# Performance work log

Measured on AMD Instinct MI355X. Metric: run time of the kernel, lower is better.

The kernel has to match this reference:

```python
import jax, jax.numpy as jnp
import numpy as np

SOFTCAP = 50.0
EPS = 1e-6
N_HEADS, D_HEAD = 16, 64


def _rms(x, w):
    return x * jax.lax.rsqrt(jnp.mean(x * x, axis=-1, keepdims=True) + EPS) * w


def _rope(x, cos, sin):
    # Faithful to source: apply_rope uses x.size(1) as the position axis, but is
    # called on (B, H, T, Dh) tensors, so positions are indexed by HEAD index.
    n = x.shape[1]
    x1, x2 = x[..., 0::2], x[..., 1::2]
    c = cos[:n][None, :, None, :]
    s = sin[:n][None, :, None, :]
    return jnp.stack([x1 * c - x2 * s, x1 * s + x2 * c], axis=-1).reshape(x.shape)


def setup_inputs() -> dict:
    key = jax.random.key(0)
    ks = jax.random.split(key, 12)
    L, D, H, Dh, Dff, V, B, T = 6, 1024, N_HEADS, D_HEAD, 4096, 32000, 1, 1024
    r = lambda k, shape: jax.random.normal(k, shape, dtype=jnp.float32) * 0.02
    return {
        'x': jax.random.randint(ks[0], (B, T), 0, V, dtype=jnp.int32),
        'embed': r(ks[1], (V, D)),
        'ln1': jnp.ones((L, D), jnp.float32),
        'Wq': r(ks[2], (L, H * Dh, D)),
        'Wk': r(ks[3], (L, H * Dh, D)),
        'Wv': r(ks[4], (L, H * Dh, D)),
        'Wo': r(ks[5], (L, D, H * Dh)),
        'qn': jnp.ones((L, Dh), jnp.float32),
        'kn': jnp.ones((L, Dh), jnp.float32),
        'ln2': jnp.ones((L, D), jnp.float32),
        'Wg': r(ks[6], (L, Dff, D)),
        'Wu': r(ks[7], (L, Dff, D)),
        'Wd': r(ks[8], (L, D, Dff)),
        'ln_out': jnp.ones((D,), jnp.float32),
    }


def reference(x, embed, ln1, Wq, Wk, Wv, Wo, qn, kn, ln2, Wg, Wu, Wd, ln_out):
    B, T = x.shape
    H, Dh = N_HEADS, D_HEAD
    scale = Dh ** -0.5
    # RoPE tables (theta=10000)
    freqs = 1.0 / (10000.0 ** (jnp.arange(0, Dh, 2, dtype=jnp.float32) / Dh))
    ang = jnp.arange(T, dtype=jnp.float32)[:, None] * freqs[None, :]
    cos, sin = jnp.cos(ang), jnp.sin(ang)
    mask = jnp.triu(jnp.ones((T, T), dtype=bool), k=1)  # True above diagonal

    h = embed[x]  # (B, T, D)

    def block(h, p):
        l1, wq, wk, wv, wo, qnw, knw, l2, wg, wu, wd = p
        hn = _rms(h, l1)
        q = (hn @ wq.T).reshape(B, T, H, Dh).transpose(0, 2, 1, 3)  # (B,H,T,Dh)
        k = (hn @ wk.T).reshape(B, T, H, Dh).transpose(0, 2, 1, 3)
        v = (hn @ wv.T).reshape(B, T, H, Dh).transpose(0, 2, 1, 3)
        q = _rope(_rms(q, qnw), cos, sin)
        k = _rope(_rms(k, knw), cos, sin)
        scores = jnp.einsum('bhtd,bhsd->bhts', q, k) * scale
        scores = SOFTCAP * jnp.tanh(scores / SOFTCAP)
        scores = jnp.where(mask[None, None], -jnp.inf, scores)
        attn = jax.nn.softmax(scores, axis=-1)
        o = jnp.einsum('bhts,bhsd->bhtd', attn, v)
        o = o.transpose(0, 2, 1, 3).reshape(B, T, H * Dh)
        h = h + o @ wo.T
        hn2 = _rms(h, l2)
        h = h + (jax.nn.silu(hn2 @ wg.T) * (hn2 @ wu.T)) @ wd.T
        return h, None

    h, _ = jax.lax.scan(block, h, (ln1, Wq, Wk, Wv, Wo, qn, kn, ln2, Wg, Wu, Wd))
    # tied embed/head
    logits = _rms(h, ln_out) @ embed.T  # (B, T, V)
    return logits
```

## Files before the change

### kernel.cpp

```cpp
#include <hip/hip_runtime.h>
#include <math.h>
#include <type_traits>

typedef __bf16 bf16_t;
typedef bf16_t bf16x4 __attribute__((ext_vector_type(4)));
typedef bf16_t bf16x8 __attribute__((ext_vector_type(8)));
typedef float  f32x4  __attribute__((ext_vector_type(4)));

#define RMS_EPS 1e-6f

enum { EP_STORE = 0, EP_RESID = 1, EP_SPLIT = 2, EP_SILU = 3, EP_QKV = 4 };

template<int V> using IC = std::integral_constant<int, V>;

static __device__ __forceinline__ f32x4 mfma16(bf16x8 a, bf16x8 b, f32x4 c) {
    return __builtin_amdgcn_mfma_f32_16x16x32_bf16(a, b, c, 0, 0, 0);
}

#define GLDS(gp, lp) __builtin_amdgcn_global_load_lds( \
    (const __attribute__((address_space(1))) void*)(gp), \
    (__attribute__((address_space(3))) void*)(lp), 16, 0, 0)

template<int N> static __device__ __forceinline__ void vmwait() {
    if constexpr (N == 0)       asm volatile("s_waitcnt vmcnt(0)" ::: "memory");
    else if constexpr (N == 2)  asm volatile("s_waitcnt vmcnt(2)" ::: "memory");
    else if constexpr (N == 3)  asm volatile("s_waitcnt vmcnt(3)" ::: "memory");
    else if constexpr (N == 4)  asm volatile("s_waitcnt vmcnt(4)" ::: "memory");
    else if constexpr (N == 6)  asm volatile("s_waitcnt vmcnt(6)" ::: "memory");
    else if constexpr (N == 8)  asm volatile("s_waitcnt vmcnt(8)" ::: "memory");
    else if constexpr (N == 12) asm volatile("s_waitcnt vmcnt(12)" ::: "memory");
    __builtin_amdgcn_sched_barrier(0);
}
static __device__ __forceinline__ void bar() { __builtin_amdgcn_s_barrier(); }
static __device__ __forceinline__ void lgkm0() {
    asm volatile("s_waitcnt lgkmcnt(0)" ::: "memory");
    __builtin_amdgcn_sched_barrier(0);
}

template<int BM, int BN, int WR, int WC, int PLANES, int EPIL, int MINW, int DEPTH>
__global__ __launch_bounds__(WR * WC * 64, MINW)
void gemm_bf16(const bf16_t* __restrict__ Ah, const bf16_t* __restrict__ Al,
               const bf16_t* __restrict__ Bh,
               float* __restrict__ Cf, bf16_t* __restrict__ Ch, bf16_t* __restrict__ Cl,
               int K, int lda, int ldb, int ldc, long long sC,
               const float* __restrict__ qnw, const float* __restrict__ knw,
               const float* __restrict__ ctab, const float* __restrict__ stab)
{
    constexpr int ASZ = BM * 32, BSZ = BN * 32;
    constexpr int NW = WR * WC;
    constexpr int NLD = (BM / 16 * (PLANES >= 2 ? 2 : 1) + BN / 16) / NW;
    __shared__ __align__(16) bf16_t sAh[DEPTH][ASZ], sBh[DEPTH][BSZ];
    __shared__ __align__(16) bf16_t sAl[PLANES >= 2 ? DEPTH : 1][PLANES >= 2 ? ASZ : 8];

    const int gx = gridDim.x;
    int id = blockIdx.x + gx * blockIdx.y;
    if (gridDim.z == 1) {
        int nwg = gx * gridDim.y;
        int q = nwg >> 3, r = nwg & 7;
        int xcd = id & 7, ix = id >> 3;
        id = (xcd < r ? xcd * (q + 1) : r * (q + 1) + (xcd - r) * q) + ix;
    }
    const int bm = id % gx, bn = id / gx;
    const int row0 = bm * BM, col0 = bn * BN;

    const size_t kofs = (size_t)blockIdx.z * K;
    Ah += kofs;  Bh += kofs;
    if constexpr (PLANES >= 2) Al += kofs;

    const int tid = threadIdx.x, lane = tid & 63, wave = tid >> 6;
    const int lr = lane & 15, lg = lane >> 4;
    constexpr int WM = BM / WR, WN = BN / WC, MF = WM / 16, NF = WN / 16;
    const int wr = wave / WC, wc = wave % WC;

    f32x4 acc[MF][NF];
    #pragma unroll
    for (int m = 0; m < MF; ++m)
        #pragma unroll
        for (int n = 0; n < NF; ++n) acc[m][n] = (f32x4){0.f, 0.f, 0.f, 0.f};

    auto stage = [&](int k0, int p) {
        #pragma unroll
        for (int i = wave; i < BM / 16; i += NW) {
            int s = i * 64 + lane, rr = s >> 2, c = s & 3;
            size_t go = (size_t)(row0 + rr) * lda + k0 + ((c ^ ((rr >> 1) & 3)) << 3);
            GLDS(Ah + go, &sAh[p][i * 512]);
            if constexpr (PLANES >= 2) GLDS(Al + go, &sAl[p][i * 512]);
        }
        #pragma unroll
        for (int i = wave; i < BN / 16; i += NW) {
            int s = i * 64 + lane, rr = s >> 2, c = s & 3;
            size_t go = (size_t)(col0 + rr) * ldb + k0 + ((c ^ ((rr >> 1) & 3)) << 3);
            GLDS(Bh + go, &sBh[p][i * 512]);
        }
    };

    auto compute = [&](int p) {
        bf16x8 ahf[MF], alf[MF], bhf[NF];
        #pragma unroll
        for (int m = 0; m < MF; ++m) {
            int rr = wr * WM + m * 16 + lr;
            int by = rr * 64 + ((lg ^ ((rr >> 1) & 3)) << 4);
            ahf[m] = *(const bf16x8*)((const char*)&sAh[p][0] + by);
            if constexpr (PLANES >= 2)
                alf[m] = *(const bf16x8*)((const char*)&sAl[p][0] + by);
        }
        #pragma unroll
        for (int n = 0; n < NF; ++n) {
            int rr = wc * WN + n * 16 + lr;
            int by = rr * 64 + ((lg ^ ((rr >> 1) & 3)) << 4);
            bhf[n] = *(const bf16x8*)((const char*)&sBh[p][0] + by);
        }
        #pragma unroll
        for (int m = 0; m < MF; ++m)
            #pragma unroll
            for (int n = 0; n < NF; ++n) {
                acc[m][n] = mfma16(ahf[m], bhf[n], acc[m][n]);
                if constexpr (PLANES >= 2)
                    acc[m][n] = mfma16(alf[m], bhf[n], acc[m][n]);
            }
    };

    if constexpr (DEPTH == 3) {
        const int NC = K >> 5;
        stage(0, 0);
        stage(32, 1);
        for (int j = 0; j + 2 < NC; ++j) {
            stage(32 * (j + 2), (j + 2) % 3);
            vmwait<2 * NLD>(); bar();
            compute(j % 3);
            bar();
        }
        vmwait<NLD>(); bar();
        compute((K >> 5) >= 2 ? ((K >> 5) - 2) % 3 : 0);
        vmwait<0>(); bar();
        compute(((K >> 5) - 1) % 3);
    } else {
        stage(0, 0);
        int k0 = 32;
        for (; k0 + 32 < K; k0 += 64) {
            stage(k0, 1);
            vmwait<NLD>(); bar();
            compute(0);
            bar();
            stage(k0 + 32, 0);
            vmwait<NLD>(); bar();
            compute(1);
            bar();
        }
        stage(k0, 1);
        vmwait<NLD>(); bar();
        compute(0);
        bar();
        vmwait<0>(); bar();
        compute(1);
    }

    if constexpr (EPIL == EP_QKV) {
        const int colbase = col0 + wc * WN;
        const int typ = colbase >> 10;
        if (typ < 2) {
            const float* nw = (typ == 0) ? qnw : knw;
            const int hh = (colbase - typ * 1024) >> 6;
            #pragma unroll
            for (int m = 0; m < MF; ++m)
                #pragma unroll
                for (int r = 0; r < 4; ++r) {
                    int grow = row0 + wr * WM + m * 16 + lg * 4 + r;
                    float ss = 0.f;
                    #pragma unroll
                    for (int n = 0; n < NF; ++n) {
                        float v = acc[m][n][r];
                        ss += v * v;
                    }
                    ss += __shfl_xor(ss, 1, 64);
                    ss += __shfl_xor(ss, 2, 64);
                    ss += __shfl_xor(ss, 4, 64);
                    ss += __shfl_xor(ss, 8, 64);
                    float inv = rsqrtf(ss * (1.0f / 64.0f) + RMS_EPS);
                    #pragma unroll
                    for (int n = 0; n < NF; ++n) {
                        int i = n * 16 + lr;
                        float x = acc[m][n][r] * inv * nw[i];
                        float p = __shfl_xor(x, 1, 64);
                        float cs = ctab[(hh << 5) + (i >> 1)];
                        float sn = stab[(hh << 5) + (i >> 1)];
                        float o = (lr & 1) ? (p * sn + x * cs) : (x * cs - p * sn);
                        Ch[(size_t)grow * ldc + colbase + i] = (bf16_t)o;
                    }
                }
        } else {
            bf16_t* vTh_ = Cl;
            bf16_t* vTl_ = (bf16_t*)Cf;
            const int vcb = colbase - 2048;
            #pragma unroll
            for (int m = 0; m < MF; ++m)
                #pragma unroll
                for (int n = 0; n < NF; ++n) {
                    int vc = vcb + n * 16 + lr;
                    int grow0 = row0 + wr * WM + m * 16 + lg * 4;
                    bf16x4 hv, lv;
                    #pragma unroll
                    for (int r = 0; r < 4; ++r) {
                        float v = acc[m][n][r];
                        bf16_t hb = (bf16_t)v;
                        hv[r] = hb;
                        lv[r] = (bf16_t)(v - (float)hb);
                    }
                    *(bf16x4*)&vTh_[(size_t)vc * 1024 + grow0] = hv;
                    *(bf16x4*)&vTl_[(size_t)vc * 1024 + grow0] = lv;
                }
        }
        return;
    }

    #pragma unroll
    for (int m = 0; m < MF; ++m)
        #pragma unroll
        for (int n = 0; n < NF; ++n)
            #pragma unroll
            for (int r = 0; r < 4; ++r) {
                int grow = row0 + wr * WM + m * 16 + lg * 4 + r;
                int gcol = col0 + wc * WN + n * 16 + lr;
                float v = acc[m][n][r];
                size_t off = (size_t)blockIdx.z * sC + (size_t)grow * ldc + gcol;
                if constexpr (EPIL == EP_STORE) {
                    Cf[off] = v;
                } else if constexpr (EPIL == EP_RESID) {
                    Cf[off] += v;
                } else if constexpr (EPIL == EP_SPLIT) {
                    bf16_t hb = (bf16_t)v;
                    Ch[off] = hb;
                    Cl[off] = (bf16_t)(v - (float)hb);
                }
            }
}

__global__ __launch_bounds__(512, 4)
void gemm_gu_pack(const bf16_t* __restrict__ Ah, const bf16_t* __restrict__ Bh,
                  bf16_t* __restrict__ Ch,
                  const float* wq, const float* wk, const float* wv,
                  const float* wo, const float* wg, const float* wu,
                  const float* wd, bf16_t* wAd, bf16_t* wGUd, bf16_t* wdd,
                  const float* __restrict__ embed, bf16_t* __restrict__ eh,
                  int es, int ee)
{
    constexpr int lda = 1024, ldb = 1024, ldc = 4096, K = 1024;
    const int tid = threadIdx.x;

    if (blockIdx.z == 2) {
        int base = ((int)blockIdx.y * 8 + (int)blockIdx.x) * 512 + tid;
        for (int j = 0; j < 11; ++j) {
            int u = es + j * 131072 + base;
            if (u < ee) {
                f32x4 v = ((const f32x4*)embed)[u];
                bf16x4 hv;
                #pragma unroll
                for (int q2 = 0; q2 < 4; ++q2) hv[q2] = (bf16_t)v[q2];
                ((bf16x4*)eh)[u] = hv;
            }
        }
        return;
    }

    if (blockIdx.z == 1) {
        if (!wq) return;
        int base = ((int)blockIdx.y * 8 + (int)blockIdx.x) * 512 + tid;
        #pragma unroll 4
        for (int j = 0; j < 32; ++j) {
            int v = j * 131072 + base;
            f32x4 val;
            bf16_t* dst;
            size_t doff;
            if (v < (1 << 20)) {
                int b = v >> 8, col = v & 255;
                const float* src = b < 1024 ? wq : b < 2048 ? wk : b < 3072 ? wv : wo;
                val = ((const f32x4*)src)[(size_t)(b & 1023) * 256 + col];
                dst = wAd; doff = (size_t)b * 256 + col;
            } else if (v < 3 * (1 << 20)) {
                int u = v - (1 << 20);
                int bb = u >> 8, col = u & 255;
                int row = bb < 4096 ? 2 * bb : 2 * (bb - 4096) + 1;
                const float* src = bb < 4096 ? wg : wu;
                val = ((const f32x4*)src)[(size_t)(bb & 4095) * 256 + col];
                dst = wGUd; doff = (size_t)row * 256 + col;
            } else {
                int u = v - 3 * (1 << 20);
                val = ((const f32x4*)wd)[u];
                dst = wdd; doff = (size_t)u;
            }
            bf16x4 hv;
            #pragma unroll
            for (int q2 = 0; q2 < 4; ++q2) hv[q2] = (bf16_t)val[q2];
            ((bf16x4*)dst)[doff] = hv;
        }
        return;
    }

    __shared__ __align__(16) bf16_t sA[3][128 * 32], sB[3][256 * 32];

    int id = blockIdx.x + 8 * blockIdx.y;
    {
        int q = 256 >> 3;
        int xcd = id & 7, ix = id >> 3;
        id = xcd * q + ix;
    }
    const int bm = id % 8, bn = id / 8;
    const int row0 = bm * 128, col0 = bn * 256;

    const int lane = tid & 63, wave = tid >> 6;
    const int lr = lane & 15, lg = lane >> 4;
    const int wr = wave >> 2, wc = wave & 3;

    f32x4 acc[4][4];
    #pragma unroll
    for (int m = 0; m < 4; ++m)
        #pragma unroll
        for (int n = 0; n < 4; ++n) acc[m][n] = (f32x4){0.f, 0.f, 0.f, 0.f};

    auto stage = [&](int k0, int p) {
        {
            int i = wave;
            int s = i * 64 + lane, rr = s >> 2, c = s & 3;
            size_t go = (size_t)(row0 + rr) * lda + k0 + ((c ^ ((rr >> 1) & 3)) << 3);
            GLDS(Ah + go, &sA[p][i * 512]);
        }
        #pragma unroll
        for (int i = wave; i < 16; i += 8) {
            int s = i * 64 + lane, rr = s >> 2, c = s & 3;
            size_t go = (size_t)(col0 + rr) * ldb + k0 + ((c ^ ((rr >> 1) & 3)) << 3);
            GLDS(Bh + go, &sB[p][i * 512]);
        }
    };

    auto compute = [&](int p) {
        bf16x8 af[4], bf4[4];
        #pragma unroll
        for (int m = 0; m < 4; ++m) {
            int rr = wr * 64 + m * 16 + lr;
            int by = rr * 64 + ((lg ^ ((rr >> 1) & 3)) << 4);
            af[m] = *(const bf16x8*)((const char*)&sA[p][0] + by);
        }
        #pragma unroll
        for (int n = 0; n < 4; ++n) {
            int rr = wc * 64 + n * 16 + lr;
            int by = rr * 64 + ((lg ^ ((rr >> 1) & 3)) << 4);
            bf4[n] = *(const bf16x8*)((const char*)&sB[p][0] + by);
        }
        #pragma unroll
        for (int m = 0; m < 4; ++m)
            #pragma unroll
            for (int n = 0; n < 4; ++n)
                acc[m][n] = mfma16(af[m], bf4[n], acc[m][n]);
    };

    const int NC = K >> 5;
    stage(0, 0);
    stage(32, 1);
    for (int j = 0; j + 2 < NC; ++j) {
        stage(32 * (j + 2), (j + 2) % 3);
        vmwait<6>(); bar();
        compute(j % 3);
        bar();
    }
    vmwait<3>(); bar();
    compute((NC - 2) % 3);
    vmwait<0>(); bar();
    compute((NC - 1) % 3);

    #pragma unroll
    for (int m = 0; m < 4; ++m)
        #pragma unroll
        for (int n = 0; n < 4; ++n)
            #pragma unroll
            for (int r = 0; r < 4; ++r) {
                int grow = row0 + wr * 64 + m * 16 + lg * 4 + r;
                int gcol = col0 + wc * 64 + n * 16 + lr;
                float v = acc[m][n][r];
                float pv = __shfl_xor(v, 1, 64);
                if (!(lr & 1)) {
                    float s = (v / (1.0f + __expf(-v))) * pv;
                    Ch[(size_t)grow * ldc + (gcol >> 1)] = (bf16_t)s;
                }
            }
}

__global__ __launch_bounds__(512, 2)
void gemm_logits8(const bf16_t* __restrict__ Ah, const bf16_t* __restrict__ Bh,
                  float* __restrict__ Cf)
{
    constexpr int lda = 1024, ldb = 1024, ldc = 32000;
    constexpr int NT = 16;
    __shared__ __align__(16) bf16_t sA[2][2][256 * 32];
    __shared__ __align__(16) bf16_t sB[2][2][256 * 32];

    const int gx = gridDim.x;
    int id = blockIdx.x + gx * blockIdx.y;
    {
        int nwg = gx * gridDim.y;
        int q = nwg >> 3, r = nwg & 7;
        int xcd = id & 7, ix = id >> 3;
        id = (xcd < r ? xcd * (q + 1) : r * (q + 1) + (xcd - r) * q) + ix;
    }
    const int bm = id % gx, bn = id / gx;
    const int row0 = bm * 256, col0 = bn * 256;

    const int tid = threadIdx.x, lane = tid & 63, wave = tid >> 6;
    const int lr = lane & 15, lg = lane >> 4;
    const int wr = wave >> 2, wc = wave & 3;

    f32x4 acc[8][4];
    #pragma unroll
    for (int m = 0; m < 8; ++m)
        #pragma unroll
        for (int n = 0; n < 4; ++n) acc[m][n] = (f32x4){0.f, 0.f, 0.f, 0.f};

    auto stageA = [&](int chunk, int buf, int ks) {
        int k0 = chunk * 32;
        #pragma unroll
        for (int i = wave; i < 16; i += 8) {
            int s = i * 64 + lane, rr = s >> 2, c = s & 3;
            size_t go = (size_t)(row0 + rr) * lda + k0 + ((c ^ ((rr >> 1) & 3)) << 3);
            GLDS(Ah + go, &sA[buf][ks][i * 512]);
        }
    };
    auto stageB = [&](int chunk, int buf, int ks) {
        int k0 = chunk * 32;
        #pragma unroll
        for (int i = wave; i < 16; i += 8) {
            int s = i * 64 + lane, rr = s >> 2, c = s & 3;
            size_t go = (size_t)(col0 + rr) * ldb + k0 + ((c ^ ((rr >> 1) & 3)) << 3);
            GLDS(Bh + go, &sB[buf][ks][i * 512]);
        }
    };

    auto phase = [&](int t, auto ksc) {
        constexpr int ks = decltype(ksc)::value;
        const int buf = t & 1;
        bf16x8 af[8], bf4[4];
        #pragma unroll
        for (int m = 0; m < 8; ++m) {
            int rr = wr * 128 + m * 16 + lr;
            int by = rr * 64 + ((lg ^ ((rr >> 1) & 3)) << 4);
            af[m] = *(const bf16x8*)((const char*)&sA[buf][ks][0] + by);
        }
        #pragma unroll
        for (int n = 0; n < 4; ++n) {
            int rr = wc * 64 + n * 16 + lr;
            int by = rr * 64 + ((lg ^ ((rr >> 1) & 3)) << 4);
            bf4[n] = *(const bf16x8*)((const char*)&sB[buf][ks][0] + by);
        }
        if constexpr (ks == 0) {
            if (t + 1 < NT) {
                stageA(2 * (t + 1) + 1, (t + 1) & 1, 1);
                stageB(2 * (t + 1) + 1, (t + 1) & 1, 1);
                vmwait<8>();
            } else {
                vmwait<0>();
            }
        } else {
            if (t + 2 < NT) {
                stageA(2 * (t + 2), t & 1, 0);
                stageB(2 * (t + 2), t & 1, 0);
                vmwait<8>();
            } else if (t + 1 < NT) {
                vmwait<4>();
            } else {
                vmwait<0>();
            }
        }
        bar();
        lgkm0();
        __builtin_amdgcn_s_setprio(1);
        #pragma unroll
        for (int m = 0; m < 8; ++m)
            #pragma unroll
            for (int n = 0; n < 4; ++n)
                acc[m][n] = mfma16(af[m], bf4[n], acc[m][n]);
        __builtin_amdgcn_s_setprio(0);
        bar();
    };

    stageA(0, 0, 0); stageB(0, 0, 0);
    stageA(1, 0, 1); stageB(1, 0, 1);
    stageA(2, 1, 0); stageB(2, 1, 0);
    vmwait<8>(); bar();

    for (int t = 0; t < NT; ++t) {
        phase(t, IC<0>{});
        phase(t, IC<1>{});
    }

    #pragma unroll
    for (int m = 0; m < 8; ++m)
        #pragma unroll
        for (int n = 0; n < 4; ++n)
            #pragma unroll
            for (int r = 0; r < 4; ++r) {
                int grow = row0 + wr * 128 + m * 16 + lg * 4 + r;
                int gcol = col0 + wc * 64 + n * 16 + lr;
                Cf[(size_t)grow * ldc + gcol] = acc[m][n][r];
            }
}

static __device__ __forceinline__ void wsplit_body(
    int b2, int tid,
    const float* wq, const float* wk, const float* wv, const float* wo,
    const float* wg, const float* wu, const float* wd,
    bf16_t* wAh, bf16_t* wGUh, bf16_t* wdh)
{
    #pragma unroll
    for (int k = 0; k < 4; ++k) {
        int b = b2 * 4 + k;
        const float* src;
        bf16_t* dst;
        size_t so, doff;
        if (b < 4096) {
            src = b < 1024 ? wq : b < 2048 ? wk : b < 3072 ? wv : wo;
            so = (size_t)(b & 1023) * 256 + tid;
            doff = (size_t)b * 256 + tid;
            dst = wAh;
        } else if (b < 12288) {
            int bb = b - 4096;
            int row = bb < 4096 ? 2 * bb : 2 * (bb - 4096) + 1;
            src = bb < 4096 ? wg : wu;
            so = (size_t)(bb & 4095) * 256 + tid;
            doff = (size_t)row * 256 + tid;
            dst = wGUh;
        } else {
            src = wd;
            so = (size_t)(b - 12288) * 256 + tid;
            doff = so;
            dst = wdh;
        }
        f32x4 v = ((const f32x4*)src)[so];
        bf16x4 hv;
        #pragma unroll
        for (int j = 0; j < 4; ++j) hv[j] = (bf16_t)v[j];
        ((bf16x4*)dst)[doff] = hv;
    }
}

__global__ __launch_bounds__(256)
void reduce_rms(const float* __restrict__ p, float* __restrict__ h,
                const float* __restrict__ w, bf16_t* __restrict__ outh)
{
    int blk = blockIdx.x, tid = threadIdx.x;
    size_t i = (size_t)blk * 256 + tid;
    const size_t S = (1024 * 1024) / 4;
    f32x4 a = ((const f32x4*)p)[i];
    f32x4 b = ((const f32x4*)p)[i + S];
    f32x4 c = ((const f32x4*)p)[i + 2 * S];
    f32x4 d = ((const f32x4*)p)[i + 3 * S];
    f32x4 hv = ((const f32x4*)h)[i];
    #pragma unroll
    for (int j = 0; j < 4; ++j) hv[j] += (a[j] + b[j]) + (c[j] + d[j]);
    ((f32x4*)h)[i] = hv;

    float ss = hv[0]*hv[0] + hv[1]*hv[1] + hv[2]*hv[2] + hv[3]*hv[3];
    #pragma unroll
    for (int m = 1; m < 64; m <<= 1) ss += __shfl_xor(ss, m, 64);
    __shared__ float red[4];
    if ((tid & 63) == 0) red[tid >> 6] = ss;
    __syncthreads();
    float tot = red[0] + red[1] + red[2] + red[3];
    float inv = rsqrtf(tot * (1.0f / 1024.0f) + RMS_EPS);
    f32x4 wt4 = *(const f32x4*)(w + tid * 4);
    bf16x4 hv4;
    #pragma unroll
    for (int j = 0; j < 4; ++j) hv4[j] = (bf16_t)(hv[j] * inv * wt4[j]);
    ((bf16x4*)outh)[i] = hv4;
}

__global__ __launch_bounds__(256)
void gather_rms_wsplit(const int* __restrict__ ids, const float* __restrict__ embed,
                       const float* __restrict__ w, float* __restrict__ h,
                       bf16_t* __restrict__ outh,
                       const float* wq, const float* wk, const float* wv,
                       const float* wo, const float* wg, const float* wu,
                       const float* wd, bf16_t* wAh, bf16_t* wGUh, bf16_t* wdh,
                       float* __restrict__ ctab, float* __restrict__ stab)
{
    int blk = blockIdx.x, tid = threadIdx.x;
    if (blk == 5120) {
        constexpr float kLogF = -0.41524101186092029f;
        for (int e = tid; e < 512; e += 256) {
            int hh = e >> 5, p0 = e & 31;
            float f = exp2f((float)p0 * kLogF);
            float ang = (float)hh * f;
            ctab[e] = cosf(ang);
            stab[e] = sinf(ang);
        }
        return;
    }
    if (blk >= 1024) {
        wsplit_body(blk - 1024, tid, wq, wk, wv, wo, wg, wu, wd, wAh, wGUh, wdh);
        return;
    }
    int row = ids[blk];
    f32x4 v = ((const f32x4*)(embed + (size_t)row * 1024))[tid];
    ((f32x4*)(h + (size_t)blk * 1024))[tid] = v;

    float ss = v[0]*v[0] + v[1]*v[1] + v[2]*v[2] + v[3]*v[3];
    #pragma unroll
    for (int m = 1; m < 64; m <<= 1) ss += __shfl_xor(ss, m, 64);
    __shared__ float red[4];
    if ((tid & 63) == 0) red[tid >> 6] = ss;
    __syncthreads();
    float tot = red[0] + red[1] + red[2] + red[3];
    float inv = rsqrtf(tot * (1.0f / 1024.0f) + RMS_EPS);
    f32x4 wt4 = *(const f32x4*)(w + tid * 4);
    bf16x4 hv;
    #pragma unroll
    for (int j = 0; j < 4; ++j) hv[j] = (bf16_t)(v[j] * inv * wt4[j]);
    ((bf16x4*)outh)[(size_t)blk * 256 + tid] = hv;
}

__global__ __launch_bounds__(128, 2)
void flash_attn(const bf16_t* __restrict__ qkvh,
                const bf16_t* __restrict__ vTh, const bf16_t* __restrict__ vTl,
                bf16_t* __restrict__ oh)
{
    __shared__ __align__(16) bf16_t sQ[32*64];
    __shared__ __align__(16) bf16_t sK[2][64*64], sVh[2][64*64], sVl[2][64*64];
    __shared__ __align__(16) bf16_t sPh[32*64], sPl[32*64];

    const int q0 = blockIdx.x * 32;
    const int hh = blockIdx.y;
    const int tid = threadIdx.x, lane = tid & 63, w = tid >> 6;
    const int lr = lane & 15, lg = lane >> 4;

    #pragma unroll
    for (int ii = 0; ii < 2; ++ii) {
        int r0 = w * 16 + ii * 8;
        int r  = r0 + (lane >> 3);
        int i  = lane & 7;
        GLDS(qkvh + (size_t)(q0 + r) * 3072 + hh * 64 + ((i ^ (r & 7)) << 3),
             sQ + r0 * 64);
    }

    auto stageKV = [&](int t, int buf) {
        const int kv0 = t * 64;
        #pragma unroll
        for (int ii = 0; ii < 4; ++ii) {
            int r0 = w * 32 + ii * 8;
            int r  = r0 + (lane >> 3);
            int i  = lane & 7;
            GLDS(qkvh + (size_t)(kv0 + r) * 3072 + 1024 + hh * 64 + ((i ^ (r & 7)) << 3),
                 sK[buf] + r0 * 64);
            GLDS(vTh + (size_t)(hh * 64 + r) * 1024 + kv0 + ((i ^ (r & 7)) << 3),
                 sVh[buf] + r0 * 64);
            GLDS(vTl + (size_t)(hh * 64 + r) * 1024 + kv0 + ((i ^ (r & 7)) << 3),
                 sVl[buf] + r0 * 64);
        }
    };

    const int ntiles = ((q0 + 31) >> 6) + 1;
    stageKV(0, 0);

    bf16x8 qa[2];
    f32x4 o_acc[4];
    #pragma unroll
    for (int n = 0; n < 4; ++n) o_acc[n] = (f32x4){0.f, 0.f, 0.f, 0.f};
    float m_run[4] = {-1e30f, -1e30f, -1e30f, -1e30f};
    float l_run[4] = {0.f, 0.f, 0.f, 0.f};

    for (int t = 0; t < ntiles; ++t) {
        const int kv0 = t * 64;
        const int buf = t & 1;
        if (t + 1 < ntiles) {
            stageKV(t + 1, buf ^ 1);
            vmwait<12>();
        } else {
            vmwait<0>();
        }
        bar();
        if (t == 0) {
            #pragma unroll
            for (int ks = 0; ks < 2; ++ks) {
                int r = w * 16 + lr;
                qa[ks] = *(const bf16x8*)((const char*)sQ + r * 128 +
                                          ((((ks << 2) | lg) ^ (r & 7)) << 4));
            }
        }

        f32x4 s_acc[4];
        #pragma unroll
        for (int n = 0; n < 4; ++n) s_acc[n] = (f32x4){0.f, 0.f, 0.f, 0.f};
        #pragma unroll
        for (int ks = 0; ks < 2; ++ks)
            #pragma unroll
            for (int n = 0; n < 4; ++n) {
                int r = n * 16 + lr;
                bf16x8 kb = *(const bf16x8*)((const char*)&sK[buf][0] + r * 128 +
                                             ((((ks << 2) | lg) ^ (r & 7)) << 4));
                s_acc[n] = mfma16(qa[ks], kb, s_acc[n]);
            }

        #pragma unroll
        for (int j = 0; j < 4; ++j) {
            int qr = q0 + w * 16 + lg * 4 + j;
            float p[4];
            float mx = -1e30f;
            #pragma unroll
            for (int n = 0; n < 4; ++n) {
                float sx = s_acc[n][j] * (0.125f * 0.02f);
                float v = 50.f * (1.f - 2.f / (1.f + __expf(2.f * sx)));
                int key = kv0 + n * 16 + lr;
                if (key > qr) v = -1e30f;
                p[n] = v;
                mx = fmaxf(mx, v);
            }
            #pragma unroll
            for (int m = 1; m < 16; m <<= 1) mx = fmaxf(mx, __shfl_xor(mx, m, 64));
            float mn = fmaxf(m_run[j], mx);
            float ef = __expf(m_run[j] - mn);
            m_run[j] = mn;
            float rs = 0.f;
            #pragma unroll
            for (int n = 0; n < 4; ++n) {
                float e = __expf(p[n] - mn);
                p[n] = e;
                rs += e;
            }
            #pragma unroll
            for (int m = 1; m < 16; m <<= 1) rs += __shfl_xor(rs, m, 64);
            l_run[j] = l_run[j] * ef + rs;
            #pragma unroll
            for (int n = 0; n < 4; ++n) o_acc[n][j] *= ef;
            int r = w * 16 + lg * 4 + j;
            #pragma unroll
            for (int n = 0; n < 4; ++n) {
                int c = n * 16 + lr;
                int byo = r * 128 + ((((c >> 3) ^ (r & 7)) << 4)) + ((c & 7) << 1);
                bf16_t hb = (bf16_t)p[n];
                *(bf16_t*)((char*)sPh + byo) = hb;
                *(bf16_t*)((char*)sPl + byo) = (bf16_t)(p[n] - (float)hb);
            }
        }

        #pragma unroll
        for (int ks = 0; ks < 2; ++ks) {
            int pr = w * 16 + lr;
            int pby = pr * 128 + ((((ks << 2) | lg) ^ (pr & 7)) << 4);
            bf16x8 pa  = *(const bf16x8*)((const char*)sPh + pby);
            bf16x8 pl_ = *(const bf16x8*)((const char*)sPl + pby);
            #pragma unroll
            for (int n = 0; n < 4; ++n) {
                int vr = n * 16 + lr;
                int vby = vr * 128 + ((((ks << 2) | lg) ^ (vr & 7)) << 4);
                bf16x8 vhf = *(const bf16x8*)((const char*)&sVh[buf][0] + vby);
                bf16x8 vlf = *(const bf16x8*)((const char*)&sVl[buf][0] + vby);
                o_acc[n] = mfma16(pa,  vhf, o_acc[n]);
                o_acc[n] = mfma16(pl_, vhf, o_acc[n]);
                o_acc[n] = mfma16(pa,  vlf, o_acc[n]);
            }
        }
        bar();
    }

    #pragma unroll
    for (int j = 0; j < 4; ++j) {
        float inv = 1.0f / l_run[j];
        int qr = q0 + w * 16 + lg * 4 + j;
        #pragma unroll
        for (int n = 0; n < 4; ++n) {
            size_t off = (size_t)qr * 1024 + hh * 64 + n * 16 + lr;
            oh[off] = (bf16_t)(o_acc[n][j] * inv);
        }
    }
}

__global__ __launch_bounds__(256)
void rmsnorm_split(const float* __restrict__ in, const float* __restrict__ w,
                   bf16_t* __restrict__ outh)
{
    int row = blockIdx.x, tid = threadIdx.x;
    f32x4 v = *(const f32x4*)(in + (size_t)row * 1024 + tid * 4);
    float ss = v[0]*v[0] + v[1]*v[1] + v[2]*v[2] + v[3]*v[3];
    #pragma unroll
    for (int m = 1; m < 64; m <<= 1) ss += __shfl_xor(ss, m, 64);
    __shared__ float red[4];
    if ((tid & 63) == 0) red[tid >> 6] = ss;
    __syncthreads();
    float tot = red[0] + red[1] + red[2] + red[3];
    float inv = rsqrtf(tot * (1.0f / 1024.0f) + RMS_EPS);
    f32x4 wt4 = *(const f32x4*)(w + tid * 4);
    bf16x4 hv;
    #pragma unroll
    for (int j = 0; j < 4; ++j) hv[j] = (bf16_t)(v[j] * inv * wt4[j]);
    ((bf16x4*)outh)[(size_t)row * 256 + tid] = hv;
}

extern "C" void kernel_launch(void* const* d_in, const int* in_sizes, int n_in,
                              void* d_out, int out_size, void* d_ws, size_t ws_size,
                              hipStream_t stream)
{
    (void)in_sizes; (void)n_in; (void)out_size; (void)ws_size;
    const int*   x_ids = (const int*)  d_in[0];
    const float* embed = (const float*)d_in[1];
    const float* ln1   = (const float*)d_in[2];
    const float* Wq    = (const float*)d_in[3];
    const float* Wk    = (const float*)d_in[4];
    const float* Wv    = (const float*)d_in[5];
    const float* Wo    = (const float*)d_in[6];
    const float* qn    = (const float*)d_in[7];
    const float* kn    = (const float*)d_in[8];
    const float* ln2   = (const float*)d_in[9];
    const float* Wg    = (const float*)d_in[10];
    const float* Wu    = (const float*)d_in[11];
    const float* Wd    = (const float*)d_in[12];
    const float* lnout = (const float*)d_in[13];
    float* out = (float*)d_out;

    char* ws = (char*)d_ws;
    const size_t MB = 1 << 20;
    float*  h    = (float*) (ws +   0 * MB);
    bf16_t* hnh  = (bf16_t*)(ws +   4 * MB);
    bf16_t* qkvh = (bf16_t*)(ws +   8 * MB);
    bf16_t* vTh  = (bf16_t*)(ws +  20 * MB);
    bf16_t* vTl  = (bf16_t*)(ws +  22 * MB);
    bf16_t* oh   = (bf16_t*)(ws +  24 * MB);
    bf16_t* wA[2]  = {(bf16_t*)(ws +  28 * MB), (bf16_t*)(ws +  84 * MB)};
    bf16_t* wGU[2] = {(bf16_t*)(ws +  36 * MB), (bf16_t*)(ws +  92 * MB)};
    bf16_t* wD[2]  = {(bf16_t*)(ws +  52 * MB), (bf16_t*)(ws + 108 * MB)};
    bf16_t* silh = (bf16_t*)(ws +  60 * MB);
    float*  wdp  = (float*) (ws +  68 * MB);
    bf16_t* eh   = (bf16_t*)(ws + 116 * MB);
    float*  ctab = (float*) (ws + 179 * MB);
    float*  stab = (float*) (ws + 179 * MB + 4096);

    const long long M1 = 1024 * 1024;
    const int ETOT = 8192000;
    const int ESL  = 1365334;

    gather_rms_wsplit<<<5121, 256, 0, stream>>>(
        x_ids, embed, ln1, h, hnh,
        Wq, Wk, Wv, Wo, Wg, Wu, Wd, wA[0], wGU[0], wD[0], ctab, stab);

    for (int l = 0; l < 6; ++l) {
        const int s = l & 1, nx = s ^ 1;

        gemm_bf16<64,128,2,2,1,EP_QKV,4,3><<<dim3(16,24),256,0,stream>>>(
            hnh, nullptr, wA[s], (float*)vTl, qkvh, vTh, 1024, 1024, 1024, 3072, 0,
            qn + l * 64, kn + l * 64, ctab, stab);

        flash_attn<<<dim3(32,16), 128, 0, stream>>>(qkvh, vTh, vTl, oh);

        gemm_bf16<64,64,2,2,1,EP_RESID,4,3><<<dim3(16,16),256,0,stream>>>(
            oh, nullptr, wA[s] + 3 * M1, h, nullptr, nullptr, 1024, 1024, 1024, 1024, 0,
            nullptr, nullptr, nullptr, nullptr);

        rmsnorm_split<<<1024, 256, 0, stream>>>(h, ln2 + l * 1024, hnh);

        int es = l * ESL, ee = (l + 1) * ESL < ETOT ? (l + 1) * ESL : ETOT;
        gemm_gu_pack<<<dim3(8,32,3), 512, 0, stream>>>(
            hnh, wGU[s], silh,
            l < 5 ? Wq + (size_t)(l+1) * M1 : nullptr,
            l < 5 ? Wk + (size_t)(l+1) * M1 : nullptr,
            l < 5 ? Wv + (size_t)(l+1) * M1 : nullptr,
            l < 5 ? Wo + (size_t)(l+1) * M1 : nullptr,
            l < 5 ? Wg + (size_t)(l+1) * 4 * M1 : nullptr,
            l < 5 ? Wu + (size_t)(l+1) * 4 * M1 : nullptr,
            l < 5 ? Wd + (size_t)(l+1) * 4 * M1 : nullptr,
            wA[nx], wGU[nx], wD[nx],
            embed, eh, es, ee);

        gemm_bf16<128,128,2,2,1,EP_STORE,4,3><<<dim3(8,8,4),256,0,stream>>>(
            silh, nullptr, wD[s], wdp, nullptr, nullptr, 1024, 4096, 4096, 1024, M1,
            nullptr, nullptr, nullptr, nullptr);

        const float* wnext = (l < 5) ? (ln1 + (l + 1) * 1024) : lnout;
        reduce_rms<<<1024, 256, 0, stream>>>(wdp, h, wnext, hnh);
    }

    gemm_logits8<<<dim3(4,125), 512, 0, stream>>>(hnh, eh, out);
}
```

Baseline: 1.040 ms.

## Fuse RMSNorm and split-K reduction into GEMM epilogues via atomic tile counters

Replaces the Wo GEMM plus separate rmsnorm kernel with one kernel. Its last tile block for each 64-row band, found with an atomic counter, computes the RMS norm and writes the bf16 normalized rows. Likewise the Wd split-K GEMM and reduce_rms kernel are merged: the last z-slice for each tile sums the partials into h, and the last tile in each row band then runs the RMS norm. This removes two kernel launches per layer and the extra passes over h. In exchange the norm runs serially inside a single block per row band, and correctness depends on threadfence and counter ordering. The generic GEMM template also drops its unused two-plane and depth-2 paths.

```diff
diff --git a/kernel.cpp b/kernel.cpp
--- a/kernel.cpp
+++ b/kernel.cpp
@@ -50,7 +50,6 @@
     constexpr int NW = WR * WC;
     constexpr int NLD = (BM / 16 * (PLANES >= 2 ? 2 : 1) + BN / 16) / NW;
     __shared__ __align__(16) bf16_t sAh[DEPTH][ASZ], sBh[DEPTH][BSZ];
-    __shared__ __align__(16) bf16_t sAl[PLANES >= 2 ? DEPTH : 1][PLANES >= 2 ? ASZ : 8];
 
     const int gx = gridDim.x;
     int id = blockIdx.x + gx * blockIdx.y;
@@ -65,7 +64,6 @@
 
     const size_t kofs = (size_t)blockIdx.z * K;
     Ah += kofs;  Bh += kofs;
-    if constexpr (PLANES >= 2) Al += kofs;
 
     const int tid = threadIdx.x, lane = tid & 63, wave = tid >> 6;
     const int lr = lane & 15, lg = lane >> 4;
@@ -84,7 +82,6 @@
             int s = i * 64 + lane, rr = s >> 2, c = s & 3;
             size_t go = (size_t)(row0 + rr) * lda + k0 + ((c ^ ((rr >> 1) & 3)) << 3);
             GLDS(Ah + go, &sAh[p][i * 512]);
-            if constexpr (PLANES >= 2) GLDS(Al + go, &sAl[p][i * 512]);
         }
         #pragma unroll
         for (int i = wave; i < BN / 16; i += NW) {
@@ -95,14 +92,12 @@
     };
 
     auto compute = [&](int p) {
-        bf16x8 ahf[MF], alf[MF], bhf[NF];
+        bf16x8 ahf[MF], bhf[NF];
         #pragma unroll
         for (int m = 0; m < MF; ++m) {
             int rr = wr * WM + m * 16 + lr;
             int by = rr * 64 + ((lg ^ ((rr >> 1) & 3)) << 4);
             ahf[m] = *(const bf16x8*)((const char*)&sAh[p][0] + by);
-            if constexpr (PLANES >= 2)
-                alf[m] = *(const bf16x8*)((const char*)&sAl[p][0] + by);
         }
         #pragma unroll
         for (int n = 0; n < NF; ++n) {
@@ -113,47 +108,23 @@
         #pragma unroll
         for (int m = 0; m < MF; ++m)
             #pragma unroll
-            for (int n = 0; n < NF; ++n) {
+            for (int n = 0; n < NF; ++n)
                 acc[m][n] = mfma16(ahf[m], bhf[n], acc[m][n]);
-                if constexpr (PLANES >= 2)
-                    acc[m][n] = mfma16(alf[m], bhf[n], acc[m][n]);
-            }
-    };
-
-    if constexpr (DEPTH == 3) {
-        const int NC = K >> 5;
-        stage(0, 0);
-        stage(32, 1);
-        for (int j = 0; j + 2 < NC; ++j) {
-            stage(32 * (j + 2), (j + 2) % 3);
-            vmwait<2 * NLD>(); bar();
-            compute(j % 3);
-            bar();
-        }
-        vmwait<NLD>(); bar();
-        compute((K >> 5) >= 2 ? ((K >> 5) - 2) % 3 : 0);
-        vmwait<0>(); bar();
-        compute(((K >> 5) - 1) % 3);
-    } else {
-        stage(0, 0);
-        int k0 = 32;
-        for (; k0 + 32 < K; k0 += 64) {
-            stage(k0, 1);
-            vmwait<NLD>(); bar();
-            compute(0);
-            bar();
-            stage(k0 + 32, 0);
-            vmwait<NLD>(); bar();
-            compute(1);
-            bar();
-        }
-        stage(k0, 1);
-        vmwait<NLD>(); bar();
-        compute(0);
+    };
+
+    const int NC = K >> 5;
+    stage(0, 0);
+    stage(32, 1);
+    for (int j = 0; j + 2 < NC; ++j) {
+        stage(32 * (j + 2), (j + 2) % 3);
+        vmwait<2 * NLD>(); bar();
+        compute(j % 3);
         bar();
-        vmwait<0>(); bar();
-        compute(1);
-    }
+    }
+    vmwait<NLD>(); bar();
+    compute((NC - 2) % 3);
+    vmwait<0>(); bar();
+    compute((NC - 1) % 3);
 
     if constexpr (EPIL == EP_QKV) {
         const int colbase = col0 + wc * WN;
@@ -212,27 +183,272 @@
         }
         return;
     }
-
-    #pragma unroll
-    for (int m = 0; m < MF; ++m)
-        #pragma unroll
-        for (int n = 0; n < NF; ++n)
+}
+
+__global__ __launch_bounds__(256, 4)
+void gemm_wo_rms(const bf16_t* __restrict__ Ah, const bf16_t* __restrict__ Bh,
+                 float* __restrict__ h, const float* __restrict__ ln2w,
+                 bf16_t* __restrict__ hnh, int* __restrict__ cnt)
+{
+    constexpr int lda = 1024, ldb = 1024, K = 1024;
+    __shared__ __align__(16) bf16_t sA[3][64 * 32], sB[3][64 * 32];
+
+    int id = blockIdx.x + 16 * blockIdx.y;
+    {
+        int xcd = id & 7, ix = id >> 3;
+        id = xcd * 32 + ix;
+    }
+    const int bm = id % 16, bn = id / 16;
+    const int row0 = bm * 64, col0 = bn * 64;
+
+    const int tid = threadIdx.x, lane = tid & 63, wave = tid >> 6;
+    const int lr = lane & 15, lg = lane >> 4;
+    const int wr = wave >> 1, wc = wave & 1;
+
+    f32x4 acc[2][2];
+    #pragma unroll
+    for (int m = 0; m < 2; ++m)
+        #pragma unroll
+        for (int n = 0; n < 2; ++n) acc[m][n] = (f32x4){0.f, 0.f, 0.f, 0.f};
+
+    auto stage = [&](int k0, int p) {
+        {
+            int i = wave;
+            int s = i * 64 + lane, rr = s >> 2, c = s & 3;
+            size_t go = (size_t)(row0 + rr) * lda + k0 + ((c ^ ((rr >> 1) & 3)) << 3);
+            GLDS(Ah + go, &sA[p][i * 512]);
+        }
+        {
+            int i = wave;
+            int s = i * 64 + lane, rr = s >> 2, c = s & 3;
+            size_t go = (size_t)(col0 + rr) * ldb + k0 + ((c ^ ((rr >> 1) & 3)) << 3);
+            GLDS(Bh + go, &sB[p][i * 512]);
+        }
+    };
+
+    auto compute = [&](int p) {
+        bf16x8 af[2], bf2[2];
+        #pragma unroll
+        for (int m = 0; m < 2; ++m) {
+            int rr = wr * 32 + m * 16 + lr;
+            int by = rr * 64 + ((lg ^ ((rr >> 1) & 3)) << 4);
+            af[m] = *(const bf16x8*)((const char*)&sA[p][0] + by);
+        }
+        #pragma unroll
+        for (int n = 0; n < 2; ++n) {
+            int rr = wc * 32 + n * 16 + lr;
+            int by = rr * 64 + ((lg ^ ((rr >> 1) & 3)) << 4);
+            bf2[n] = *(const bf16x8*)((const char*)&sB[p][0] + by);
+        }
+        #pragma unroll
+        for (int m = 0; m < 2; ++m)
+            #pragma unroll
+            for (int n = 0; n < 2; ++n)
+                acc[m][n] = mfma16(af[m], bf2[n], acc[m][n]);
+    };
+
+    const int NC = K >> 5;
+    stage(0, 0);
+    stage(32, 1);
+    for (int j = 0; j + 2 < NC; ++j) {
+        stage(32 * (j + 2), (j + 2) % 3);
+        vmwait<4>(); bar();
+        compute(j % 3);
+        bar();
+    }
+    vmwait<2>(); bar();
+    compute((NC - 2) % 3);
+    vmwait<0>(); bar();
+    compute((NC - 1) % 3);
+
+    #pragma unroll
+    for (int m = 0; m < 2; ++m)
+        #pragma unroll
+        for (int n = 0; n < 2; ++n)
             #pragma unroll
             for (int r = 0; r < 4; ++r) {
-                int grow = row0 + wr * WM + m * 16 + lg * 4 + r;
-                int gcol = col0 + wc * WN + n * 16 + lr;
-                float v = acc[m][n][r];
-                size_t off = (size_t)blockIdx.z * sC + (size_t)grow * ldc + gcol;
-                if constexpr (EPIL == EP_STORE) {
-                    Cf[off] = v;
-                } else if constexpr (EPIL == EP_RESID) {
-                    Cf[off] += v;
-                } else if constexpr (EPIL == EP_SPLIT) {
-                    bf16_t hb = (bf16_t)v;
-                    Ch[off] = hb;
-                    Cl[off] = (bf16_t)(v - (float)hb);
-                }
-            }
+                int grow = row0 + wr * 32 + m * 16 + lg * 4 + r;
+                int gcol = col0 + wc * 32 + n * 16 + lr;
+                h[(size_t)grow * 1024 + gcol] += acc[m][n][r];
+            }
+
+    __shared__ int tk;
+    __syncthreads();
+    if (tid == 0) {
+        __threadfence();
+        tk = atomicAdd(&cnt[bm], 1);
+    }
+    __syncthreads();
+    if (tk == 15) {
+        if (tid == 0) __threadfence();
+        __syncthreads();
+        int r = tid >> 2, sub = tid & 3;
+        const f32x4* hr = (const f32x4*)(h + (size_t)(row0 + r) * 1024) + sub * 64;
+        float ss = 0.f;
+        for (int k = 0; k < 64; ++k) {
+            f32x4 v = hr[k];
+            ss += v[0]*v[0] + v[1]*v[1] + v[2]*v[2] + v[3]*v[3];
+        }
+        ss += __shfl_xor(ss, 1, 64);
+        ss += __shfl_xor(ss, 2, 64);
+        float inv = rsqrtf(ss * (1.0f / 1024.0f) + RMS_EPS);
+        const f32x4* wv = (const f32x4*)ln2w + sub * 64;
+        bf16x4* dst = (bf16x4*)(hnh + (size_t)(row0 + r) * 1024) + sub * 64;
+        for (int k = 0; k < 64; ++k) {
+            f32x4 v = hr[k], wt = wv[k];
+            bf16x4 hv;
+            #pragma unroll
+            for (int j = 0; j < 4; ++j) hv[j] = (bf16_t)(v[j] * inv * wt[j]);
+            dst[k] = hv;
+        }
+        if (tid == 0) atomicExch(&cnt[bm], 0);
+    }
+}
+
+__global__ __launch_bounds__(256, 4)
+void gemm_wd_red(const bf16_t* __restrict__ Ah, const bf16_t* __restrict__ Bh,
+                 float* __restrict__ wdp, float* __restrict__ h,
+                 const float* __restrict__ wnext, bf16_t* __restrict__ hnh,
+                 int* __restrict__ cntT, int* __restrict__ cntR)
+{
+    constexpr int lda = 4096, ldb = 4096, K = 1024;
+    __shared__ __align__(16) bf16_t sA[3][128 * 32], sB[3][128 * 32];
+
+    const int bm = blockIdx.x, bn = blockIdx.y, z = blockIdx.z;
+    const int row0 = bm * 128, col0 = bn * 128;
+
+    const bf16_t* A = Ah + (size_t)z * K;
+    const bf16_t* B = Bh + (size_t)z * K;
+
+    const int tid = threadIdx.x, lane = tid & 63, wave = tid >> 6;
+    const int lr = lane & 15, lg = lane >> 4;
+    const int wr = wave >> 1, wc = wave & 1;
+
+    f32x4 acc[4][4];
+    #pragma unroll
+    for (int m = 0; m < 4; ++m)
+        #pragma unroll
+        for (int n = 0; n < 4; ++n) acc[m][n] = (f32x4){0.f, 0.f, 0.f, 0.f};
+
+    auto stage = [&](int k0, int p) {
+        #pragma unroll
+        for (int i = wave; i < 8; i += 4) {
+            int s = i * 64 + lane, rr = s >> 2, c = s & 3;
+            size_t go = (size_t)(row0 + rr) * lda + k0 + ((c ^ ((rr >> 1) & 3)) << 3);
+            GLDS(A + go, &sA[p][i * 512]);
+        }
+        #pragma unroll
+        for (int i = wave; i < 8; i += 4) {
+            int s = i * 64 + lane, rr = s >> 2, c = s & 3;
+            size_t go = (size_t)(col0 + rr) * ldb + k0 + ((c ^ ((rr >> 1) & 3)) << 3);
+            GLDS(B + go, &sB[p][i * 512]);
+        }
+    };
+
+    auto compute = [&](int p) {
+        bf16x8 af[4], bf4[4];
+        #pragma unroll
+        for (int m = 0; m < 4; ++m) {
+            int rr = wr * 64 + m * 16 + lr;
+            int by = rr * 64 + ((lg ^ ((rr >> 1) & 3)) << 4);
+            af[m] = *(const bf16x8*)((const char*)&sA[p][0] + by);
+        }
+        #pragma unroll
+        for (int n = 0; n < 4; ++n) {
+            int rr = wc * 64 + n * 16 + lr;
+            int by = rr * 64 + ((lg ^ ((rr >> 1) & 3)) << 4);
+            bf4[n] = *(const bf16x8*)((const char*)&sB[p][0] + by);
+        }
+        #pragma unroll
+        for (int m = 0; m < 4; ++m)
+            #pragma unroll
+            for (int n = 0; n < 4; ++n)
+                acc[m][n] = mfma16(af[m], bf4[n], acc[m][n]);
+    };
+
+    const int NC = K >> 5;
+    stage(0, 0);
+    stage(32, 1);
+    for (int j = 0; j + 2 < NC; ++j) {
+        stage(32 * (j + 2), (j + 2) % 3);
+        vmwait<8>(); bar();
+        compute(j % 3);
+        bar();
+    }
+    vmwait<4>(); bar();
+    compute((NC - 2) % 3);
+    vmwait<0>(); bar();
+    compute((NC - 1) % 3);
+
+    #pragma unroll
+    for (int m = 0; m < 4; ++m)
+        #pragma unroll
+        for (int n = 0; n < 4; ++n)
+            #pragma unroll
+            for (int r = 0; r < 4; ++r) {
+                int grow = row0 + wr * 64 + m * 16 + lg * 4 + r;
+                int gcol = col0 + wc * 64 + n * 16 + lr;
+                wdp[(size_t)z * 1048576 + (size_t)grow * 1024 + gcol] = acc[m][n][r];
+            }
+
+    __shared__ int tk, tk2;
+    const int tix = bm * 8 + bn;
+    __syncthreads();
+    if (tid == 0) {
+        __threadfence();
+        tk = atomicAdd(&cntT[tix], 1);
+    }
+    __syncthreads();
+    if (tk != 3) return;
+
+    if (tid == 0) __threadfence();
+    __syncthreads();
+    const f32x4* p4 = (const f32x4*)wdp;
+    f32x4* h4 = (f32x4*)h;
+    const int S = 262144;
+    #pragma unroll
+    for (int k = 0; k < 16; ++k) {
+        int u = tid + k * 256;
+        int r = u >> 5, c4 = u & 31;
+        size_t gi = (size_t)(row0 + r) * 256 + (col0 >> 2) + c4;
+        f32x4 a = p4[gi], b = p4[gi + S], c = p4[gi + 2 * S], d = p4[gi + 3 * S];
+        f32x4 hv = h4[gi];
+        #pragma unroll
+        for (int j = 0; j < 4; ++j) hv[j] += (a[j] + b[j]) + (c[j] + d[j]);
+        h4[gi] = hv;
+    }
+    __syncthreads();
+    if (tid == 0) {
+        atomicExch(&cntT[tix], 0);
+        __threadfence();
+        tk2 = atomicAdd(&cntR[bm], 1);
+    }
+    __syncthreads();
+    if (tk2 != 7) return;
+
+    if (tid == 0) __threadfence();
+    __syncthreads();
+    {
+        int r = tid >> 1, half = tid & 1;
+        const f32x4* hr = (const f32x4*)(h + (size_t)(row0 + r) * 1024) + half * 128;
+        float ss = 0.f;
+        for (int k = 0; k < 128; ++k) {
+            f32x4 v = hr[k];
+            ss += v[0]*v[0] + v[1]*v[1] + v[2]*v[2] + v[3]*v[3];
+        }
+        ss += __shfl_xor(ss, 1, 64);
+        float inv = rsqrtf(ss * (1.0f / 1024.0f) + RMS_EPS);
+        const f32x4* wv = (const f32x4*)wnext + half * 128;
+        bf16x4* dst = (bf16x4*)(hnh + (size_t)(row0 + r) * 1024) + half * 128;
+        for (int k = 0; k < 128; ++k) {
+            f32x4 v = hr[k], wt = wv[k];
+            bf16x4 hv;
+            #pragma unroll
+            for (int j = 0; j < 4; ++j) hv[j] = (bf16_t)(v[j] * inv * wt[j]);
+            dst[k] = hv;
+        }
+    }
+    if (tid == 0) atomicExch(&cntR[bm], 0);
 }
 
 __global__ __launch_bounds__(512, 4)
@@ -541,44 +757,14 @@
 }
 
 __global__ __launch_bounds__(256)
-void reduce_rms(const float* __restrict__ p, float* __restrict__ h,
-                const float* __restrict__ w, bf16_t* __restrict__ outh)
-{
-    int blk = blockIdx.x, tid = threadIdx.x;
-    size_t i = (size_t)blk * 256 + tid;
-    const size_t S = (1024 * 1024) / 4;
-    f32x4 a = ((const f32x4*)p)[i];
-    f32x4 b = ((const f32x4*)p)[i + S];
-    f32x4 c = ((const f32x4*)p)[i + 2 * S];
-    f32x4 d = ((const f32x4*)p)[i + 3 * S];
-    f32x4 hv = ((const f32x4*)h)[i];
-    #pragma unroll
-    for (int j = 0; j < 4; ++j) hv[j] += (a[j] + b[j]) + (c[j] + d[j]);
-    ((f32x4*)h)[i] = hv;
-
-    float ss = hv[0]*hv[0] + hv[1]*hv[1] + hv[2]*hv[2] + hv[3]*hv[3];
-    #pragma unroll
-    for (int m = 1; m < 64; m <<= 1) ss += __shfl_xor(ss, m, 64);
-    __shared__ float red[4];
-    if ((tid & 63) == 0) red[tid >> 6] = ss;
-    __syncthreads();
-    float tot = red[0] + red[1] + red[2] + red[3];
-    float inv = rsqrtf(tot * (1.0f / 1024.0f) + RMS_EPS);
-    f32x4 wt4 = *(const f32x4*)(w + tid * 4);
-    bf16x4 hv4;
-    #pragma unroll
-    for (int j = 0; j < 4; ++j) hv4[j] = (bf16_t)(hv[j] * inv * wt4[j]);
-    ((bf16x4*)outh)[i] = hv4;
-}
-
-__global__ __launch_bounds__(256)
 void gather_rms_wsplit(const int* __restrict__ ids, const float* __restrict__ embed,
                        const float* __restrict__ w, float* __restrict__ h,
                        bf16_t* __restrict__ outh,
                        const float* wq, const float* wk, const float* wv,
                        const float* wo, const float* wg, const float* wu,
                        const float* wd, bf16_t* wAh, bf16_t* wGUh, bf16_t* wdh,
-                       float* __restrict__ ctab, float* __restrict__ stab)
+                       float* __restrict__ ctab, float* __restrict__ stab,
+                       int* __restrict__ cnts)
 {
     int blk = blockIdx.x, tid = threadIdx.x;
     if (blk == 5120) {
@@ -590,6 +776,7 @@
             ctab[e] = cosf(ang);
             stab[e] = sinf(ang);
         }
+        if (tid < 88) atomicExch(&cnts[tid], 0);
         return;
     }
     if (blk >= 1024) {
@@ -768,27 +955,6 @@
             oh[off] = (bf16_t)(o_acc[n][j] * inv);
         }
     }
-}
-
-__global__ __launch_bounds__(256)
-void rmsnorm_split(const float* __restrict__ in, const float* __restrict__ w,
-                   bf16_t* __restrict__ outh)
-{
-    int row = blockIdx.x, tid = threadIdx.x;
-    f32x4 v = *(const f32x4*)(in + (size_t)row * 1024 + tid * 4);
-    float ss = v[0]*v[0] + v[1]*v[1] + v[2]*v[2] + v[3]*v[3];
-    #pragma unroll
-    for (int m = 1; m < 64; m <<= 1) ss += __shfl_xor(ss, m, 64);
-    __shared__ float red[4];
-    if ((tid & 63) == 0) red[tid >> 6] = ss;
-    __syncthreads();
-    float tot = red[0] + red[1] + red[2] + red[3];
-    float inv = rsqrtf(tot * (1.0f / 1024.0f) + RMS_EPS);
-    f32x4 wt4 = *(const f32x4*)(w + tid * 4);
-    bf16x4 hv;
-    #pragma unroll
-    for (int j = 0; j < 4; ++j) hv[j] = (bf16_t)(v[j] * inv * wt4[j]);
-    ((bf16x4*)outh)[(size_t)row * 256 + tid] = hv;
 }
 
 extern "C" void kernel_launch(void* const* d_in, const int* in_sizes, int n_in,
@@ -828,6 +994,7 @@
     bf16_t* eh   = (bf16_t*)(ws + 116 * MB);
     float*  ctab = (float*) (ws + 179 * MB);
     float*  stab = (float*) (ws + 179 * MB + 4096);
+    int*    cnts = (int*)   (ws + 179 * MB + 8192);
 
     const long long M1 = 1024 * 1024;
     const int ETOT = 8192000;
@@ -835,7 +1002,7 @@
 
     gather_rms_wsplit<<<5121, 256, 0, stream>>>(
         x_ids, embed, ln1, h, hnh,
-        Wq, Wk, Wv, Wo, Wg, Wu, Wd, wA[0], wGU[0], wD[0], ctab, stab);
+        Wq, Wk, Wv, Wo, Wg, Wu, Wd, wA[0], wGU[0], wD[0], ctab, stab, cnts);
 
     for (int l = 0; l < 6; ++l) {
         const int s = l & 1, nx = s ^ 1;
@@ -846,11 +1013,8 @@
 
         flash_attn<<<dim3(32,16), 128, 0, stream>>>(qkvh, vTh, vTl, oh);
 
-        gemm_bf16<64,64,2,2,1,EP_RESID,4,3><<<dim3(16,16),256,0,stream>>>(
-            oh, nullptr, wA[s] + 3 * M1, h, nullptr, nullptr, 1024, 1024, 1024, 1024, 0,
-            nullptr, nullptr, nullptr, nullptr);
-
-        rmsnorm_split<<<1024, 256, 0, stream>>>(h, ln2 + l * 1024, hnh);
+        gemm_wo_rms<<<dim3(16,16), 256, 0, stream>>>(
+            oh, wA[s] + 3 * M1, h, ln2 + l * 1024, hnh, cnts);
 
         int es = l * ESL, ee = (l + 1) * ESL < ETOT ? (l + 1) * ESL : ETOT;
         gemm_gu_pack<<<dim3(8,32,3), 512, 0, stream>>>(
@@ -865,12 +1029,9 @@
             wA[nx], wGU[nx], wD[nx],
             embed, eh, es, ee);
 
-        gemm_bf16<128,128,2,2,1,EP_STORE,4,3><<<dim3(8,8,4),256,0,stream>>>(
-            silh, nullptr, wD[s], wdp, nullptr, nullptr, 1024, 4096, 4096, 1024, M1,
-            nullptr, nullptr, nullptr, nullptr);
-
         const float* wnext = (l < 5) ? (ln1 + (l + 1) * 1024) : lnout;
-        reduce_rms<<<1024, 256, 0, stream>>>(wdp, h, wnext, hnh);
+        gemm_wd_red<<<dim3(8,8,4), 256, 0, stream>>>(
+            silh, wD[s], wdp, h, wnext, hnh, cnts + 16, cnts + 80);
     }
 
     gemm_logits8<<<dim3(4,125), 512, 0, stream>>>(hnh, eh, out);
```

After: 1.526 ms. 46.8% more time.
